# Kernel tuning notes

Hardware: AMD Instinct MI355X
Metric: run time of the kernel (lower is better)

Reference implementation:

```python
import jax, jax.numpy as jnp
import numpy as np
from jax import lax

B, S, D, H = 256, 1024, 64, 128


def setup_inputs() -> dict:
    key = jax.random.key(0)
    ks = jax.random.split(key, 11)
    s_in = 1.0 / np.sqrt(H)  # torch RNNCell/Linear init scale (uniform bound); normal scale ok for testing
    return {
        "inputs": jax.random.normal(ks[0], (B, S, D), jnp.float32),
        "Wih_fw": jax.random.normal(ks[1], (H, D), jnp.float32) * s_in,
        "Whh_fw": jax.random.normal(ks[2], (H, H), jnp.float32) * s_in,
        "bih_fw": jax.random.normal(ks[3], (H,), jnp.float32) * s_in,
        "bhh_fw": jax.random.normal(ks[4], (H,), jnp.float32) * s_in,
        "Wih_bw": jax.random.normal(ks[5], (H, D), jnp.float32) * s_in,
        "Whh_bw": jax.random.normal(ks[6], (H, H), jnp.float32) * s_in,
        "bih_bw": jax.random.normal(ks[7], (H,), jnp.float32) * s_in,
        "bhh_bw": jax.random.normal(ks[8], (H,), jnp.float32) * s_in,
        "fc_W": jax.random.normal(ks[9], (1, 2 * H), jnp.float32) * (1.0 / np.sqrt(2 * H)),
        "fc_b": jnp.zeros((1,), jnp.float32),
    }


def _run_dir(inputs, Wih, Whh, bih, bhh, reverse):
    # Precompute input projection for all timesteps: [B,S,H]
    xp = jnp.einsum('bsd,hd->bsh', inputs, Wih) + bih + bhh
    WhhT = Whh.T

    def step(h, x_t):  # x_t: [B,H]
        h_new = jnp.tanh(x_t + h @ WhhT)
        return h_new, h_new

    h0 = jnp.zeros((inputs.shape[0], Whh.shape[0]), inputs.dtype)
    # scan over time; reverse=True processes t = S-1..0 and emits outputs in
    # original time order, matching torch's output_bw[::-1] stacking.
    _, ys = lax.scan(step, h0, jnp.swapaxes(xp, 0, 1), reverse=reverse)
    return jnp.swapaxes(ys, 0, 1)  # [B,S,H]


def reference(inputs, Wih_fw, Whh_fw, bih_fw, bhh_fw,
              Wih_bw, Whh_bw, bih_bw, bhh_bw, fc_W, fc_b):
    out_fw = _run_dir(inputs, Wih_fw, Whh_fw, bih_fw, bhh_fw, reverse=False)
    out_bw = _run_dir(inputs, Wih_bw, Whh_bw, bih_bw, bhh_bw, reverse=True)
    outputs = jnp.concatenate([out_fw, out_bw], axis=2)  # [B,S,2H]
    outputs = outputs @ fc_W.T + fc_b  # [B,S,1]
    return jnp.squeeze(outputs, -1)  # [B,S]
```

## Files before the change

### kernel.cpp

```cpp
#include <hip/hip_runtime.h>

namespace {

constexpr int kS = 1024;
constexpr int kD = 64;
constexpr int kH = 128;

typedef __attribute__((ext_vector_type(2))) _Float16 half2v;
typedef __attribute__((ext_vector_type(4))) float f32x4;
typedef __attribute__((ext_vector_type(8))) _Float16 half8;

__device__ __forceinline__ float fdot2(unsigned w, unsigned h, float acc) {
#if __has_builtin(__builtin_amdgcn_fdot2)
  return __builtin_amdgcn_fdot2(__builtin_bit_cast(half2v, w),
                                __builtin_bit_cast(half2v, h), acc, false);
#else
  float d;
  asm("v_dot2_f32_f16 %0, %1, %2, %3" : "=v"(d) : "v"(w), "v"(h), "v"(acc));
  return d;
#endif
}

__device__ __forceinline__ unsigned bcast(unsigned v, int k) {
  return (unsigned)__builtin_amdgcn_ds_bpermute(4 * k, (int)v);
}

__device__ __forceinline__ unsigned pk16(float a, float b) {
  half2v h;
  h.x = (_Float16)a;
  h.y = (_Float16)b;
  return __builtin_bit_cast(unsigned, h);
}

__device__ __forceinline__ float fast_tanh(float x) {
#if __has_builtin(__builtin_amdgcn_fmed3f)
  x = __builtin_amdgcn_fmed3f(x, -15.f, 15.f);
#else
  x = fminf(fmaxf(x, -15.f), 15.f);
#endif
  float e = __expf(2.f * x);
  return (e - 1.f) * __builtin_amdgcn_rcpf(e + 1.f);
}

#if __has_builtin(__builtin_amdgcn_mov_dpp)
__device__ __forceinline__ float lane_xor1(float v) {
  return __int_as_float(__builtin_amdgcn_mov_dpp(__float_as_int(v), 0xB1, 0xF, 0xF, true));
}
#else
__device__ __forceinline__ float lane_xor1(float v) {
  return __int_as_float(__builtin_amdgcn_ds_swizzle(__float_as_int(v), 0x041F));
}
#endif

__device__ __forceinline__ void stage_chunk(const char* g, unsigned* lds, int L) {
#pragma unroll
  for (int k = 0; k < 8; ++k) {
    __builtin_amdgcn_global_load_lds(
        (const __attribute__((address_space(1))) void*)(g + k * 1024 + L * 16),
        (__attribute__((address_space(3))) void*)(lds + k * 256), 16, 0, 0);
  }
}


__global__ __launch_bounds__(256, 2) void xproj_kernel(
    const float* __restrict__ inputs,
    const float* __restrict__ Wih_fw, const float* __restrict__ bih_fw,
    const float* __restrict__ bhh_fw,
    const float* __restrict__ Wih_bw, const float* __restrict__ bih_bw,
    const float* __restrict__ bhh_bw,
    _Float16* __restrict__ xp) {
  __shared__ _Float16 Wl[256 * 80];
  __shared__ _Float16 xl[128 * 80];
  __shared__ float biasl[256];

  const int tid = threadIdx.x;
  const int b = blockIdx.x;
  const int w = tid >> 6;
  const int lane = tid & 63;
  const int n16 = lane & 15;
  const int q = lane >> 4;

  {
    const int jd = tid;
    const float* src = (jd < kH) ? (Wih_fw + jd * kD) : (Wih_bw + (jd - kH) * kD);
    const float4* s4 = (const float4*)src;
#pragma unroll
    for (int k = 0; k < 8; ++k) {
      float4 a = s4[2 * k], c = s4[2 * k + 1];
      half8 h;
      h[0] = (_Float16)a.x; h[1] = (_Float16)a.y; h[2] = (_Float16)a.z; h[3] = (_Float16)a.w;
      h[4] = (_Float16)c.x; h[5] = (_Float16)c.y; h[6] = (_Float16)c.z; h[7] = (_Float16)c.w;
      *(half8*)&Wl[jd * 80 + k * 8] = h;
    }
    biasl[jd] = (jd < kH) ? (bih_fw[jd] + bhh_fw[jd])
                          : (bih_bw[jd - kH] + bhh_bw[jd - kH]);
  }

  for (int ch = 0; ch < 8; ++ch) {
    __syncthreads();
    {
      const int tl = tid >> 1, hf = tid & 1;
      const float4* s4 = (const float4*)(inputs +
          ((size_t)b * kS + ch * 128 + tl) * kD + hf * 32);
#pragma unroll
      for (int k = 0; k < 4; ++k) {
        float4 a = s4[2 * k], c = s4[2 * k + 1];
        half8 h;
        h[0] = (_Float16)a.x; h[1] = (_Float16)a.y; h[2] = (_Float16)a.z; h[3] = (_Float16)a.w;
        h[4] = (_Float16)c.x; h[5] = (_Float16)c.y; h[6] = (_Float16)c.z; h[7] = (_Float16)c.w;
        *(half8*)&xl[tl * 80 + hf * 32 + k * 8] = h;
      }
    }
    __syncthreads();

    half8 bf0[4], bf1[4];
    float bs[4];
#pragma unroll
    for (int nn = 0; nn < 4; ++nn) {
      const int jd = (w * 4 + nn) * 16 + n16;
      bf0[nn] = *(const half8*)&Wl[jd * 80 + q * 8];
      bf1[nn] = *(const half8*)&Wl[jd * 80 + q * 8 + 32];
      bs[nn] = biasl[jd];
    }

#pragma unroll 2
    for (int m = 0; m < 8; ++m) {
      const int trow = m * 16 + n16;
      const half8 a0 = *(const half8*)&xl[trow * 80 + q * 8];
      const half8 a1 = *(const half8*)&xl[trow * 80 + q * 8 + 32];
#pragma unroll
      for (int nn = 0; nn < 4; ++nn) {
        f32x4 acc = {0.f, 0.f, 0.f, 0.f};
        acc = __builtin_amdgcn_mfma_f32_16x16x32_f16(a0, bf0[nn], acc, 0, 0, 0);
        acc = __builtin_amdgcn_mfma_f32_16x16x32_f16(a1, bf1[nn], acc, 0, 0, 0);
        const int jd = (w * 4 + nn) * 16 + n16;
        const int dir = jd >> 7, j = jd & 127;
        const size_t slab = (size_t)(dir * 256 + b) * (kS * kH);
#pragma unroll
        for (int r = 0; r < 4; ++r) {
          const int t = ch * 128 + m * 16 + q * 4 + r;
          const int tt = dir ? (kS - 1 - t) : t;
          xp[slab + (size_t)(tt >> 5) * (32 * kH) + (tt & 31) * kH + j] =
              (_Float16)(acc[r] + bs[nn]);
        }
      }
    }
  }
}

__global__ __launch_bounds__(64, 1) void birnn_step_kernel(
    const _Float16* __restrict__ xp,
    const float* __restrict__ Whh_fw, const float* __restrict__ Whh_bw,
    const float* __restrict__ fcW, const float* __restrict__ fcb,
    float* __restrict__ out) {
  const int dir = blockIdx.x >> 8;
  const int b = blockIdx.x & 255;
  const int L = threadIdx.x;

  __shared__ unsigned jrn[32 * 68];
  __shared__ unsigned xbuf[2][2048];
  __shared__ unsigned fcwl[64];
  __shared__ float outbuf[kS];

  const float* __restrict__ Whh = dir ? Whh_bw : Whh_fw;

  unsigned w0[64], w1[64];
  {
    const float* r0 = Whh + (size_t)(2 * L) * kH;
    const float* r1 = Whh + (size_t)(2 * L + 1) * kH;
#pragma unroll
    for (int k = 0; k < 64; ++k) {
      w0[k] = pk16(r0[2 * k], r0[2 * k + 1]);
      w1[k] = pk16(r1[2 * k], r1[2 * k + 1]);
    }
  }
  fcwl[L] = pk16(fcW[dir * kH + 2 * L], fcW[dir * kH + 2 * L + 1]);

  unsigned hcur = 0;

  const char* slab = (const char*)(xp + (size_t)(dir * 256 + b) * (kS * kH));
  stage_chunk(slab, &xbuf[0][0], L);
  stage_chunk(slab + 8192, &xbuf[1][0], L);
  asm volatile("s_waitcnt vmcnt(0)" ::: "memory");

  for (int c = 0; c < 32; ++c) {
    const unsigned* xb = &xbuf[c & 1][0];

#pragma unroll 2
    for (int s = 0; s < 32; ++s) {
      const unsigned xdw = xb[s * 64 + L];
      float a0 = 0.f, a1 = 0.f, a2 = 0.f, a3 = 0.f;
      float c0 = 0.f, c1 = 0.f, c2 = 0.f, c3 = 0.f;

      unsigned hb[32];
#pragma unroll
      for (int k = 0; k < 32; ++k) hb[k] = bcast(hcur, k);
#pragma unroll
      for (int k = 0; k < 32; ++k) {
        a0 = fdot2(w0[k], hb[k], a0);
        c0 = fdot2(w1[k], hb[k], c0);
      }
#pragma unroll
      for (int k = 0; k < 32; ++k) hb[k] = bcast(hcur, 32 + k);
#pragma unroll
      for (int k = 0; k < 32; ++k) {
        a1 = fdot2(w0[32 + k], hb[k], a1);
        c1 = fdot2(w1[32 + k], hb[k], c1);
      }
      (void)a2; (void)a3; (void)c2; (void)c3;

      const half2v xh = __builtin_bit_cast(half2v, xdw);
      const float va = (a0 + a1) + (float)xh.x;
      const float vb = (c0 + c1) + (float)xh.y;
      hcur = pk16(fast_tanh(va), fast_tanh(vb));
      jrn[s * 68 + L] = hcur;
    }

    {
      const int tl = L >> 1, jh = L & 1;
      const uint4* rp = (const uint4*)&jrn[tl * 68 + jh * 32];
      const uint4* fp = (const uint4*)&fcwl[jh * 32];
      float acc = 0.f;
#pragma unroll
      for (int k = 0; k < 8; ++k) {
        const uint4 hv = rp[k];
        const uint4 fw = fp[k];
        acc = fdot2(fw.x, hv.x, acc);
        acc = fdot2(fw.y, hv.y, acc);
        acc = fdot2(fw.z, hv.z, acc);
        acc = fdot2(fw.w, hv.w, acc);
      }
      acc += lane_xor1(acc);
      if (jh == 0) outbuf[c * 32 + tl] = acc;
    }

    if (c < 30) {
      stage_chunk(slab + (size_t)(c + 2) * 8192, &xbuf[c & 1][0], L);
      asm volatile("s_waitcnt vmcnt(8)" ::: "memory");
    } else if (c == 30) {
      asm volatile("s_waitcnt vmcnt(0)" ::: "memory");
    }
  }

  const float fcb0 = (dir == 0) ? fcb[0] : 0.f;
#pragma unroll
  for (int k = 0; k < 16; ++k) {
    const int t = L + 64 * k;
    const int td = dir ? (kS - 1 - t) : t;
    atomicAdd(&out[(size_t)b * kS + td], outbuf[t] + fcb0);
  }
}

}

extern "C" void kernel_launch(void* const* d_in, const int* in_sizes, int n_in,
                              void* d_out, int out_size, void* d_ws, size_t ws_size,
                              hipStream_t stream) {
  (void)in_sizes; (void)n_in; (void)ws_size;
  const float* inputs = (const float*)d_in[0];
  const float* Wih_fw = (const float*)d_in[1];
  const float* Whh_fw = (const float*)d_in[2];
  const float* bih_fw = (const float*)d_in[3];
  const float* bhh_fw = (const float*)d_in[4];
  const float* Wih_bw = (const float*)d_in[5];
  const float* Whh_bw = (const float*)d_in[6];
  const float* bih_bw = (const float*)d_in[7];
  const float* bhh_bw = (const float*)d_in[8];
  const float* fc_W   = (const float*)d_in[9];
  const float* fc_b   = (const float*)d_in[10];
  float* out = (float*)d_out;
  _Float16* xpw = (_Float16*)d_ws;

  hipMemsetAsync(out, 0, (size_t)out_size * sizeof(float), stream);

  hipLaunchKernelGGL(xproj_kernel, dim3(256), dim3(256), 0, stream,
                     inputs, Wih_fw, bih_fw, bhh_fw, Wih_bw, bih_bw, bhh_bw, xpw);
  hipLaunchKernelGGL(birnn_step_kernel, dim3(512), dim3(64), 0, stream,
                     xpw, Whh_fw, Whh_bw, fc_W, fc_b, out);
}
```

Before: 567.6 us.

## Split recurrent matvec between MFMA and dot2 paths per timestep

Each timestep's recurrent product is split in two. The first half of the hidden dimension is computed with MFMA 16x16x32 f16 instructions that read the previous hidden state from the LDS journal, and the second half keeps the dot2 path with lane broadcasts. Lane-to-unit ownership is remapped so each lane can pick its MFMA output via selects. This halves the bpermute and dot2 work on the serial critical path, at the cost of an LDS round-trip per step, MFMA latency, extra registers and the removal of the unroll pragma.

```diff
diff --git a/kernel.cpp b/kernel.cpp
--- a/kernel.cpp
+++ b/kernel.cpp
@@ -59,6 +59,10 @@
         (const __attribute__((address_space(1))) void*)(g + k * 1024 + L * 16),
         (__attribute__((address_space(3))) void*)(lds + k * 256), 16, 0, 0);
   }
+}
+
+__host__ __device__ constexpr int owner_lane(int d) {
+  return 16 * ((d & 7) >> 1) + 2 * (d >> 3) + (d & 1);
 }
 
 
@@ -156,6 +160,12 @@
   const int dir = blockIdx.x >> 8;
   const int b = blockIdx.x & 255;
   const int L = threadIdx.x;
+  const int n16 = L & 15;
+  const int q = L >> 4;
+  const int t8 = (L >> 1) & 7;
+  const int e = L & 1;
+  const int dL = 8 * t8 + 2 * q + e;
+  const int u0 = 2 * dL;
 
   __shared__ unsigned jrn[32 * 68];
   __shared__ unsigned xbuf[2][2048];
@@ -164,19 +174,35 @@
 
   const float* __restrict__ Whh = dir ? Whh_bw : Whh_fw;
 
-  unsigned w0[64], w1[64];
+  half8 Afr[8][2];
+#pragma unroll
+  for (int jm = 0; jm < 8; ++jm) {
+#pragma unroll
+    for (int tk = 0; tk < 2; ++tk) {
+      const float* src = Whh + (size_t)(16 * jm + n16) * kH + 32 * tk + 8 * q;
+      const float4 a = *(const float4*)src;
+      const float4 c = *(const float4*)(src + 4);
+      half8 h;
+      h[0] = (_Float16)a.x; h[1] = (_Float16)a.y; h[2] = (_Float16)a.z; h[3] = (_Float16)a.w;
+      h[4] = (_Float16)c.x; h[5] = (_Float16)c.y; h[6] = (_Float16)c.z; h[7] = (_Float16)c.w;
+      Afr[jm][tk] = h;
+    }
+  }
+  unsigned w0v[32], w1v[32];
   {
-    const float* r0 = Whh + (size_t)(2 * L) * kH;
-    const float* r1 = Whh + (size_t)(2 * L + 1) * kH;
-#pragma unroll
-    for (int k = 0; k < 64; ++k) {
-      w0[k] = pk16(r0[2 * k], r0[2 * k + 1]);
-      w1[k] = pk16(r1[2 * k], r1[2 * k + 1]);
+    const float* r0 = Whh + (size_t)u0 * kH + 64;
+    const float* r1 = Whh + (size_t)(u0 + 1) * kH + 64;
+#pragma unroll
+    for (int g = 0; g < 32; ++g) {
+      w0v[g] = pk16(r0[2 * g], r0[2 * g + 1]);
+      w1v[g] = pk16(r1[2 * g], r1[2 * g + 1]);
     }
   }
   fcwl[L] = pk16(fcW[dir * kH + 2 * L], fcW[dir * kH + 2 * L + 1]);
+  jrn[31 * 68 + L] = 0;
 
   unsigned hcur = 0;
+  const f32x4 zeroq = {0.f, 0.f, 0.f, 0.f};
 
   const char* slab = (const char*)(xp + (size_t)(dir * 256 + b) * (kS * kH));
   stage_chunk(slab, &xbuf[0][0], L);
@@ -186,34 +212,49 @@
   for (int c = 0; c < 32; ++c) {
     const unsigned* xb = &xbuf[c & 1][0];
 
-#pragma unroll 2
     for (int s = 0; s < 32; ++s) {
-      const unsigned xdw = xb[s * 64 + L];
-      float a0 = 0.f, a1 = 0.f, a2 = 0.f, a3 = 0.f;
-      float c0 = 0.f, c1 = 0.f, c2 = 0.f, c3 = 0.f;
-
+      const int prev = (s + 31) & 31;
+      const uint4 B0 = *(const uint4*)&jrn[prev * 68 + 4 * q];
+      const uint4 B1 = *(const uint4*)&jrn[prev * 68 + 16 + 4 * q];
       unsigned hb[32];
 #pragma unroll
-      for (int k = 0; k < 32; ++k) hb[k] = bcast(hcur, k);
-#pragma unroll
-      for (int k = 0; k < 32; ++k) {
-        a0 = fdot2(w0[k], hb[k], a0);
-        c0 = fdot2(w1[k], hb[k], c0);
+      for (int g = 0; g < 32; ++g) hb[g] = bcast(hcur, owner_lane(32 + g));
+      const unsigned xdw = xb[s * 64 + dL];
+
+      const half8 b0f = __builtin_bit_cast(half8, B0);
+      const half8 b1f = __builtin_bit_cast(half8, B1);
+      f32x4 Cacc[8];
+#pragma unroll
+      for (int jm = 0; jm < 8; ++jm)
+        Cacc[jm] = __builtin_amdgcn_mfma_f32_16x16x32_f16(Afr[jm][0], b0f, zeroq, 0, 0, 0);
+#pragma unroll
+      for (int jm = 0; jm < 8; ++jm)
+        Cacc[jm] = __builtin_amdgcn_mfma_f32_16x16x32_f16(Afr[jm][1], b1f, Cacc[jm], 0, 0, 0);
+
+      float a0 = 0.f, a1 = 0.f, c0 = 0.f, c1 = 0.f;
+#pragma unroll
+      for (int g = 0; g < 16; ++g) {
+        a0 = fdot2(w0v[g], hb[g], a0);
+        c0 = fdot2(w1v[g], hb[g], c0);
+        a1 = fdot2(w0v[16 + g], hb[16 + g], a1);
+        c1 = fdot2(w1v[16 + g], hb[16 + g], c1);
       }
-#pragma unroll
-      for (int k = 0; k < 32; ++k) hb[k] = bcast(hcur, 32 + k);
-#pragma unroll
-      for (int k = 0; k < 32; ++k) {
-        a1 = fdot2(w0[32 + k], hb[k], a1);
-        c1 = fdot2(w1[32 + k], hb[k], c1);
-      }
-      (void)a2; (void)a3; (void)c2; (void)c3;
+
+      const f32x4 T01 = (t8 & 1) ? Cacc[1] : Cacc[0];
+      const f32x4 T23 = (t8 & 1) ? Cacc[3] : Cacc[2];
+      const f32x4 T45 = (t8 & 1) ? Cacc[5] : Cacc[4];
+      const f32x4 T67 = (t8 & 1) ? Cacc[7] : Cacc[6];
+      const f32x4 U0 = (t8 & 2) ? T23 : T01;
+      const f32x4 U1 = (t8 & 2) ? T67 : T45;
+      const f32x4 Q = (t8 & 4) ? U1 : U0;
+      const float s0 = e ? Q[2] : Q[0];
+      const float s1 = e ? Q[3] : Q[1];
 
       const half2v xh = __builtin_bit_cast(half2v, xdw);
-      const float va = (a0 + a1) + (float)xh.x;
-      const float vb = (c0 + c1) + (float)xh.y;
+      const float va = s0 + (a0 + a1) + (float)xh.x;
+      const float vb = s1 + (c0 + c1) + (float)xh.y;
       hcur = pk16(fast_tanh(va), fast_tanh(vb));
-      jrn[s * 68 + L] = hcur;
+      jrn[s * 68 + dL] = hcur;
     }
 
     {
```

New measurement: 703.7 us. 1.24x slower.

## Fuse input projection into recurrent kernel, computing chunks on the fly with MFMA

Applied to the files above, without the earlier changes.

Removes the separate xproj kernel and its large fp16 workspace. Each recurrent block now streams raw fp32 input chunks into LDS with async global-to-LDS loads. It computes the 32-timestep projection slice with MFMA into LDS, reversing rows for the backward direction, and adds the bias inside the step. This removes a full HBM write and read-back of the projected activations and one kernel launch. In exchange, the projection MFMAs and extra registers for Wih fragments move into the latency-bound recurrent kernel, between chunks.

```diff
diff --git a/kernel.cpp b/kernel.cpp
--- a/kernel.cpp
+++ b/kernel.cpp
@@ -32,6 +32,13 @@
   return __builtin_bit_cast(unsigned, h);
 }
 
+__device__ __forceinline__ half8 to_h8(float4 a, float4 c) {
+  half8 h;
+  h[0] = (_Float16)a.x; h[1] = (_Float16)a.y; h[2] = (_Float16)a.z; h[3] = (_Float16)a.w;
+  h[4] = (_Float16)c.x; h[5] = (_Float16)c.y; h[6] = (_Float16)c.z; h[7] = (_Float16)c.w;
+  return h;
+}
+
 __device__ __forceinline__ float fast_tanh(float x) {
 #if __has_builtin(__builtin_amdgcn_fmed3f)
   x = __builtin_amdgcn_fmed3f(x, -15.f, 15.f);
@@ -61,108 +68,31 @@
   }
 }
 
-
-__global__ __launch_bounds__(256, 2) void xproj_kernel(
+__global__ __launch_bounds__(64, 1) void birnn_fused_kernel(
     const float* __restrict__ inputs,
     const float* __restrict__ Wih_fw, const float* __restrict__ bih_fw,
     const float* __restrict__ bhh_fw,
     const float* __restrict__ Wih_bw, const float* __restrict__ bih_bw,
     const float* __restrict__ bhh_bw,
-    _Float16* __restrict__ xp) {
-  __shared__ _Float16 Wl[256 * 80];
-  __shared__ _Float16 xl[128 * 80];
-  __shared__ float biasl[256];
-
-  const int tid = threadIdx.x;
-  const int b = blockIdx.x;
-  const int w = tid >> 6;
-  const int lane = tid & 63;
-  const int n16 = lane & 15;
-  const int q = lane >> 4;
-
-  {
-    const int jd = tid;
-    const float* src = (jd < kH) ? (Wih_fw + jd * kD) : (Wih_bw + (jd - kH) * kD);
-    const float4* s4 = (const float4*)src;
-#pragma unroll
-    for (int k = 0; k < 8; ++k) {
-      float4 a = s4[2 * k], c = s4[2 * k + 1];
-      half8 h;
-      h[0] = (_Float16)a.x; h[1] = (_Float16)a.y; h[2] = (_Float16)a.z; h[3] = (_Float16)a.w;
-      h[4] = (_Float16)c.x; h[5] = (_Float16)c.y; h[6] = (_Float16)c.z; h[7] = (_Float16)c.w;
-      *(half8*)&Wl[jd * 80 + k * 8] = h;
-    }
-    biasl[jd] = (jd < kH) ? (bih_fw[jd] + bhh_fw[jd])
-                          : (bih_bw[jd - kH] + bhh_bw[jd - kH]);
-  }
-
-  for (int ch = 0; ch < 8; ++ch) {
-    __syncthreads();
-    {
-      const int tl = tid >> 1, hf = tid & 1;
-      const float4* s4 = (const float4*)(inputs +
-          ((size_t)b * kS + ch * 128 + tl) * kD + hf * 32);
-#pragma unroll
-      for (int k = 0; k < 4; ++k) {
-        float4 a = s4[2 * k], c = s4[2 * k + 1];
-        half8 h;
-        h[0] = (_Float16)a.x; h[1] = (_Float16)a.y; h[2] = (_Float16)a.z; h[3] = (_Float16)a.w;
-        h[4] = (_Float16)c.x; h[5] = (_Float16)c.y; h[6] = (_Float16)c.z; h[7] = (_Float16)c.w;
-        *(half8*)&xl[tl * 80 + hf * 32 + k * 8] = h;
-      }
-    }
-    __syncthreads();
-
-    half8 bf0[4], bf1[4];
-    float bs[4];
-#pragma unroll
-    for (int nn = 0; nn < 4; ++nn) {
-      const int jd = (w * 4 + nn) * 16 + n16;
-      bf0[nn] = *(const half8*)&Wl[jd * 80 + q * 8];
-      bf1[nn] = *(const half8*)&Wl[jd * 80 + q * 8 + 32];
-      bs[nn] = biasl[jd];
-    }
-
-#pragma unroll 2
-    for (int m = 0; m < 8; ++m) {
-      const int trow = m * 16 + n16;
-      const half8 a0 = *(const half8*)&xl[trow * 80 + q * 8];
-      const half8 a1 = *(const half8*)&xl[trow * 80 + q * 8 + 32];
-#pragma unroll
-      for (int nn = 0; nn < 4; ++nn) {
-        f32x4 acc = {0.f, 0.f, 0.f, 0.f};
-        acc = __builtin_amdgcn_mfma_f32_16x16x32_f16(a0, bf0[nn], acc, 0, 0, 0);
-        acc = __builtin_amdgcn_mfma_f32_16x16x32_f16(a1, bf1[nn], acc, 0, 0, 0);
-        const int jd = (w * 4 + nn) * 16 + n16;
-        const int dir = jd >> 7, j = jd & 127;
-        const size_t slab = (size_t)(dir * 256 + b) * (kS * kH);
-#pragma unroll
-        for (int r = 0; r < 4; ++r) {
-          const int t = ch * 128 + m * 16 + q * 4 + r;
-          const int tt = dir ? (kS - 1 - t) : t;
-          xp[slab + (size_t)(tt >> 5) * (32 * kH) + (tt & 31) * kH + j] =
-              (_Float16)(acc[r] + bs[nn]);
-        }
-      }
-    }
-  }
-}
-
-__global__ __launch_bounds__(64, 1) void birnn_step_kernel(
-    const _Float16* __restrict__ xp,
     const float* __restrict__ Whh_fw, const float* __restrict__ Whh_bw,
     const float* __restrict__ fcW, const float* __restrict__ fcb,
     float* __restrict__ out) {
   const int dir = blockIdx.x >> 8;
   const int b = blockIdx.x & 255;
   const int L = threadIdx.x;
-
+  const int n16 = L & 15;
+  const int q = L >> 4;
+
+  __shared__ float instage[2][2048];
+  __shared__ unsigned xcomp[32 * 68];
   __shared__ unsigned jrn[32 * 68];
-  __shared__ unsigned xbuf[2][2048];
   __shared__ unsigned fcwl[64];
   __shared__ float outbuf[kS];
 
   const float* __restrict__ Whh = dir ? Whh_bw : Whh_fw;
+  const float* __restrict__ Wih = dir ? Wih_bw : Wih_fw;
+  const float* __restrict__ bihd = dir ? bih_bw : bih_fw;
+  const float* __restrict__ bhhd = dir ? bhh_bw : bhh_fw;
 
   unsigned w0[64], w1[64];
   {
@@ -174,23 +104,62 @@
       w1[k] = pk16(r1[2 * k], r1[2 * k + 1]);
     }
   }
+  half8 AW[8][2];
+#pragma unroll
+  for (int m = 0; m < 8; ++m) {
+#pragma unroll
+    for (int tk = 0; tk < 2; ++tk) {
+      const float* src = Wih + (size_t)(16 * m + n16) * kD + 32 * tk + 8 * q;
+      AW[m][tk] = to_h8(*(const float4*)src, *(const float4*)(src + 4));
+    }
+  }
+  const float bj0 = bihd[2 * L] + bhhd[2 * L];
+  const float bj1 = bihd[2 * L + 1] + bhhd[2 * L + 1];
   fcwl[L] = pk16(fcW[dir * kH + 2 * L], fcW[dir * kH + 2 * L + 1]);
 
   unsigned hcur = 0;
-
-  const char* slab = (const char*)(xp + (size_t)(dir * 256 + b) * (kS * kH));
-  stage_chunk(slab, &xbuf[0][0], L);
-  stage_chunk(slab + 8192, &xbuf[1][0], L);
-  asm volatile("s_waitcnt vmcnt(0)" ::: "memory");
+  const f32x4 zeroq = {0.f, 0.f, 0.f, 0.f};
+
+  auto buildx = [&](const float* stg) {
+    half8 Bf[2][2];
+#pragma unroll
+    for (int n = 0; n < 2; ++n) {
+      const int r_loc = dir ? (31 - (16 * n + n16)) : (16 * n + n16);
+      const float* rp = stg + r_loc * 64;
+#pragma unroll
+      for (int tk = 0; tk < 2; ++tk) {
+        const float* p = rp + 32 * tk + 8 * q;
+        Bf[n][tk] = to_h8(*(const float4*)p, *(const float4*)(p + 4));
+      }
+    }
+#pragma unroll
+    for (int n = 0; n < 2; ++n) {
+      const int t_loc = 16 * n + n16;
+      unsigned* wbase = &xcomp[t_loc * 68];
+#pragma unroll
+      for (int m = 0; m < 8; ++m) {
+        f32x4 Cq = __builtin_amdgcn_mfma_f32_16x16x32_f16(AW[m][0], Bf[n][0], zeroq, 0, 0, 0);
+        Cq = __builtin_amdgcn_mfma_f32_16x16x32_f16(AW[m][1], Bf[n][1], Cq, 0, 0, 0);
+        uint2 pw;
+        pw.x = pk16(Cq[0], Cq[1]);
+        pw.y = pk16(Cq[2], Cq[3]);
+        *(uint2*)(wbase + 8 * m + 2 * q) = pw;
+      }
+    }
+  };
+
+  const char* islab = (const char*)(inputs + (size_t)b * kS * kD);
+  const int c0off = dir ? 992 : 0;
+  stage_chunk(islab + (size_t)(dir ? (c0off - 0) : 0) * 256, (unsigned*)&instage[0][0], L);
+  stage_chunk(islab + (size_t)(dir ? (c0off - 32) : 32) * 256, (unsigned*)&instage[1][0], L);
+  asm volatile("s_waitcnt vmcnt(8)" ::: "memory");
+  buildx(&instage[0][0]);
 
   for (int c = 0; c < 32; ++c) {
-    const unsigned* xb = &xbuf[c & 1][0];
-
 #pragma unroll 2
     for (int s = 0; s < 32; ++s) {
-      const unsigned xdw = xb[s * 64 + L];
-      float a0 = 0.f, a1 = 0.f, a2 = 0.f, a3 = 0.f;
-      float c0 = 0.f, c1 = 0.f, c2 = 0.f, c3 = 0.f;
+      const unsigned xdw = xcomp[s * 68 + L];
+      float a0 = 0.f, a1 = 0.f, c0 = 0.f, c1 = 0.f;
 
       unsigned hb[32];
 #pragma unroll
@@ -207,11 +176,10 @@
         a1 = fdot2(w0[32 + k], hb[k], a1);
         c1 = fdot2(w1[32 + k], hb[k], c1);
       }
-      (void)a2; (void)a3; (void)c2; (void)c3;
 
       const half2v xh = __builtin_bit_cast(half2v, xdw);
-      const float va = (a0 + a1) + (float)xh.x;
-      const float vb = (c0 + c1) + (float)xh.y;
+      const float va = (a0 + a1) + ((float)xh.x + bj0);
+      const float vb = (c0 + c1) + ((float)xh.y + bj1);
       hcur = pk16(fast_tanh(va), fast_tanh(vb));
       jrn[s * 68 + L] = hcur;
     }
@@ -235,10 +203,13 @@
     }
 
     if (c < 30) {
-      stage_chunk(slab + (size_t)(c + 2) * 8192, &xbuf[c & 1][0], L);
+      const int g2 = dir ? (c0off - 32 * (c + 2)) : 32 * (c + 2);
+      stage_chunk(islab + (size_t)g2 * 256, (unsigned*)&instage[c & 1][0], L);
       asm volatile("s_waitcnt vmcnt(8)" ::: "memory");
+      buildx(&instage[(c + 1) & 1][0]);
     } else if (c == 30) {
       asm volatile("s_waitcnt vmcnt(0)" ::: "memory");
+      buildx(&instage[1][0]);
     }
   }
 
@@ -256,7 +227,7 @@
 extern "C" void kernel_launch(void* const* d_in, const int* in_sizes, int n_in,
                               void* d_out, int out_size, void* d_ws, size_t ws_size,
                               hipStream_t stream) {
-  (void)in_sizes; (void)n_in; (void)ws_size;
+  (void)in_sizes; (void)n_in; (void)d_ws; (void)ws_size;
   const float* inputs = (const float*)d_in[0];
   const float* Wih_fw = (const float*)d_in[1];
   const float* Whh_fw = (const float*)d_in[2];
@@ -269,12 +240,10 @@
   const float* fc_W   = (const float*)d_in[9];
   const float* fc_b   = (const float*)d_in[10];
   float* out = (float*)d_out;
-  _Float16* xpw = (_Float16*)d_ws;
 
   hipMemsetAsync(out, 0, (size_t)out_size * sizeof(float), stream);
 
-  hipLaunchKernelGGL(xproj_kernel, dim3(256), dim3(256), 0, stream,
-                     inputs, Wih_fw, bih_fw, bhh_fw, Wih_bw, bih_bw, bhh_bw, xpw);
-  hipLaunchKernelGGL(birnn_step_kernel, dim3(512), dim3(64), 0, stream,
-                     xpw, Whh_fw, Whh_bw, fc_W, fc_b, out);
-}
+  hipLaunchKernelGGL(birnn_fused_kernel, dim3(512), dim3(64), 0, stream,
+                     inputs, Wih_fw, bih_fw, bhh_fw, Wih_bw, bih_bw, bhh_bw,
+                     Whh_fw, Whh_bw, fc_W, fc_b, out);
+}
```

Result: no change. 566.7 us (-0.2%).
